# Optimization experiments

Hardware: AMD Instinct MI355X
Metric: run time of the kernel (lower is better)

## Reference

```python
import jax, jax.numpy as jnp
import numpy as np

BS, C, H, W = 4, 128, 64, 64  # input_dim=128
INNER = 64


def setup_inputs() -> dict:
    key = jax.random.key(0)
    ks = jax.random.split(key, 9)
    s_in = 1.0 / np.sqrt(C)
    s_inner = 1.0 / np.sqrt(INNER)
    return {
        "inpt": jax.random.normal(ks[0], (BS, C, H, W), dtype=jnp.float32),
        "Wq": jax.random.normal(ks[1], (INNER, C), dtype=jnp.float32) * s_in,
        "bq": jax.random.normal(ks[2], (INNER,), dtype=jnp.float32) * 0.01,
        "Wk": jax.random.normal(ks[3], (INNER, C), dtype=jnp.float32) * s_in,
        "bk": jax.random.normal(ks[4], (INNER,), dtype=jnp.float32) * 0.01,
        "Wv": jax.random.normal(ks[5], (INNER, C), dtype=jnp.float32) * s_in,
        "bv": jax.random.normal(ks[6], (INNER,), dtype=jnp.float32) * 0.01,
        "Wo": jax.random.normal(ks[7], (C, INNER), dtype=jnp.float32) * s_inner,
        "bo": jax.random.normal(ks[8], (C,), dtype=jnp.float32) * 0.01,
    }


def reference(inpt, Wq, bq, Wk, bk, Wv, bv, Wo, bo):
    bs, c, h, w = inpt.shape
    L = h * w
    # [bs, C, H, W] -> [bs, L, C] (tokens = spatial positions)
    x = inpt.reshape(bs, c, L).transpose(0, 2, 1)
    q = jnp.einsum('blc,dc->bld', x, Wq) + bq  # [bs, L, INNER]
    k = jnp.einsum('blc,dc->bld', x, Wk) + bk
    v = jnp.einsum('blc,dc->bld', x, Wv) + bv
    # torch code divides by np.round(sqrt(d), 2); for d=64 this is exactly 8.0
    scale = jnp.float32(np.round(np.sqrt(q.shape[-1]), 2))
    scores = jnp.einsum('bld,bmd->blm', q, k) / scale  # [bs, L, L] score matrix
    factors = jax.nn.softmax(scores, axis=-1)
    ctx = jnp.einsum('blm,bmd->bld', factors, v)  # [bs, L, INNER]
    out = jnp.einsum('bld,cd->blc', ctx, Wo) + bo  # [bs, L, C]
    out = out.transpose(0, 2, 1).reshape(bs, c, h, w)
    return inpt + out
```

## Files before the change

### kernel.cpp

```cpp
#include <hip/hip_runtime.h>
#include <hip/hip_bf16.h>

typedef __bf16 bf16x8 __attribute__((ext_vector_type(8)));
typedef __bf16 bf16x4 __attribute__((ext_vector_type(4)));
typedef short  s16x4  __attribute__((ext_vector_type(4)));
typedef float  f32x4  __attribute__((ext_vector_type(4)));

#define MFMA32(a, b, c) __builtin_amdgcn_mfma_f32_16x16x32_bf16((a), (b), (c), 0, 0, 0)
#define MFMA16K(a, b, c) __builtin_amdgcn_mfma_f32_16x16x16bf16_1k((a), (b), (c), 0, 0, 0)

#if __has_builtin(__builtin_amdgcn_exp2f)
#define EXP2F(x) __builtin_amdgcn_exp2f(x)
#else
#define EXP2F(x) __expf(0.6931471805599453f * (x))
#endif

#define GL16(G, L)                                                            \
    __builtin_amdgcn_global_load_lds(                                         \
        (const __attribute__((address_space(1))) void*)(G),                   \
        (__attribute__((address_space(3))) void*)(L), 16, 0, 0)

#define SPLIT 8
#define QSCALE 0.18033688011112042f
#define BBOUND 12.0f


__global__ __launch_bounds__(256) void wprep_kernel(
    const float* __restrict__ Wq, const float* __restrict__ Wk,
    const float* __restrict__ Wv, const float* __restrict__ Wo,
    __bf16* __restrict__ Wqkv_b, __bf16* __restrict__ Wo_b)
{
    const int idx = (blockIdx.x * 256 + threadIdx.x) * 4;
    const float* src;
    __bf16* dst;
    if (idx < 8192)       { src = Wq + idx;         dst = Wqkv_b + idx; }
    else if (idx < 16384) { src = Wk + idx - 8192;  dst = Wqkv_b + idx; }
    else if (idx < 24576) { src = Wv + idx - 16384; dst = Wqkv_b + idx; }
    else                  { src = Wo + idx - 24576; dst = Wo_b + idx - 24576; }
    float4 v = *(const float4*)src;
    bf16x4 o;
    o[0] = (__bf16)v.x; o[1] = (__bf16)v.y;
    o[2] = (__bf16)v.z; o[3] = (__bf16)v.w;
    *(bf16x4*)dst = o;
}

__global__ __launch_bounds__(256, 4) void qkv_kernel(
    const float* __restrict__ inpt,
    const float* __restrict__ bq, const float* __restrict__ bk,
    const float* __restrict__ bv,
    const __bf16* __restrict__ Wqkv_b,
    __bf16* __restrict__ Qws, __bf16* __restrict__ Kws, __bf16* __restrict__ VTws)
{
    __shared__ __align__(16) __bf16 xT[64 * 136];
    __shared__ __align__(16) __bf16 os[64 * 136];
    const int bid = blockIdx.x;
    const int b   = bid >> 6;
    const int l0  = (bid & 63) << 6;
    const int t   = threadIdx.x;

    {
        const int c = t >> 1, half = t & 1;
        const float* xin = inpt + ((size_t)(b * 128 + c)) * 4096 + l0 + half * 32;
        #pragma unroll
        for (int i = 0; i < 8; ++i) {
            float4 v = *(const float4*)(xin + i * 4);
            const int tok = half * 32 + i * 4;
            xT[(tok + 0) * 136 + c] = (__bf16)v.x;
            xT[(tok + 1) * 136 + c] = (__bf16)v.y;
            xT[(tok + 2) * 136 + c] = (__bf16)v.z;
            xT[(tok + 3) * 136 + c] = (__bf16)v.w;
        }
    }
    __syncthreads();

    const int w    = t >> 6;
    const int lane = t & 63;
    const int quad = lane >> 4;
    const int l15  = lane & 15;

    f32x4 acc[12];
    #pragma unroll
    for (int j = 0; j < 12; ++j)
        #pragma unroll
        for (int r = 0; r < 4; ++r) acc[j][r] = 0.f;

    #pragma unroll
    for (int ks = 0; ks < 4; ++ks) {
        bf16x8 af = *(const bf16x8*)&xT[(w * 16 + l15) * 136 + ks * 32 + quad * 8];
        #pragma unroll
        for (int j = 0; j < 12; ++j) {
            bf16x8 bf = *(const bf16x8*)(Wqkv_b + j * 2048 + l15 * 128
                                         + ks * 32 + quad * 8);
            acc[j] = MFMA32(af, bf, acc[j]);
        }
    }

    #pragma unroll
    for (int j = 0; j < 12; ++j) {
        const int msel = j >> 2;
        const int o0   = (j & 3) * 16;
        const float* bb = (msel == 0) ? bq : ((msel == 1) ? bk : bv);
        float bias = bb[o0 + l15];
        if (msel < 2) {
            const float scl = (msel == 0) ? QSCALE : 1.0f;
            const int oc = j * 16 + l15;
            #pragma unroll
            for (int r = 0; r < 4; ++r)
                os[(w * 16 + quad * 4 + r) * 136 + oc]
                    = (__bf16)((acc[j][r] + bias) * scl);
        } else {
            const int d  = o0 + l15;
            const int kt = bid & 63;
            bf16x4 v;
            #pragma unroll
            for (int r = 0; r < 4; ++r) v[r] = (__bf16)(acc[j][r] + bias);
            *(bf16x4*)(VTws + (size_t)b * 262144 + kt * 4096
                       + d * 64 + quad * 16 + w * 4) = v;
        }
    }
    __syncthreads();

    #pragma unroll
    for (int g = 0; g < 4; ++g) {
        const int cid = t + g * 256;
        const int tok = cid >> 4, c8 = cid & 15;
        bf16x8 v = *(const bf16x8*)&os[tok * 136 + c8 * 8];
        if (c8 < 8) {
            *(bf16x8*)(Qws + ((size_t)(b * 4096 + l0 + tok)) * 64 + c8 * 8) = v;
        } else {
            const int d8 = c8 - 8;
            __bf16* dst = Kws + (size_t)b * 262144
                + (bid & 63) * 4096
                + (tok >> 4) * 1024
                + (d8 >> 2) * 512
                + (d8 & 3) * 128
                + (tok & 15) * 8;
            *(bf16x8*)dst = v;
        }
    }
}

__global__ __launch_bounds__(256, 4) void attn_kernel(
    const __bf16* __restrict__ Qws, const __bf16* __restrict__ Kws,
    const __bf16* __restrict__ VTws,
    __bf16* __restrict__ Ops, float* __restrict__ Lws)
{
    __shared__ __align__(16) __bf16 sbuf[2][8192];

    const int bid0  = blockIdx.x;
    const int bid   = (bid0 & 7) * 128 + (bid0 >> 3);
    const int split = bid >> 7;
    const int qi    = bid & 127;
    const int b  = qi >> 5;
    const int l0 = (qi & 31) << 7;
    const int t    = threadIdx.x;
    const int w    = t >> 6;
    const int lane = t & 63;
    const int quad = lane >> 4;
    const int l15  = lane & 15;

    bf16x8 qf[2][2];
    #pragma unroll
    for (int qs = 0; qs < 2; ++qs) {
        const __bf16* qptr = Qws
            + ((size_t)(b * 4096 + l0 + w * 32 + qs * 16 + l15)) * 64 + quad * 8;
        qf[qs][0] = *(const bf16x8*)qptr;
        qf[qs][1] = *(const bf16x8*)(qptr + 32);
    }

    f32x4 cfr[2][4];
    #pragma unroll
    for (int qs = 0; qs < 2; ++qs)
        #pragma unroll
        for (int mt = 0; mt < 4; ++mt)
            #pragma unroll
            for (int r = 0; r < 4; ++r) cfr[qs][mt][r] = 0.f;
    float l_acc[2] = {0.f, 0.f};

    int voff[8];
    #pragma unroll
    for (int mt = 0; mt < 4; ++mt) {
        const int d = mt * 16 + l15;
        #pragma unroll
        for (int kc8 = 0; kc8 < 2; ++kc8)
            voff[kc8 * 4 + mt] = d * 64 + (((2 * quad + kc8) ^ (d & 7)) * 8);
    }

    const uint4* Vg = (const uint4*)(VTws + ((size_t)b << 18));
    const int rw = t >> 3, cw = (t & 7) ^ ((t >> 3) & 7);
    const uint4* vbase = Vg + rw * 8 + cw + split * 4096;
    const uint4* kbase = (const uint4*)(Kws + ((size_t)b << 18))
                       + t + split * 4096;

    union B4 { bf16x4 h; s16x4 s; };
    union V8 { bf16x8 v; s16x4 q[2]; };

    auto stage = [&](int kt, int slot) {
        __bf16* Kd = &sbuf[slot][0];
        __bf16* Vd = &sbuf[slot][4096];
        const uint4* kp = kbase + kt * 512;
        const uint4* vp = vbase + kt * 512;
        GL16(kp,       Kd +        w * 512);
        GL16(kp + 256, Kd + 2048 + w * 512);
        GL16(vp,       Vd +        w * 512);
        GL16(vp + 256, Vd + 2048 + w * 512);
    };

    auto tile_step = [&](int slot) {
        const __bf16* Kb = &sbuf[slot][0];
        const __bf16* Vb = &sbuf[slot][4096];
        B4 pk[2][4];
        #pragma unroll
        for (int nt = 0; nt < 4; ++nt) {
            bf16x8 k0 = *(const bf16x8*)(Kb + nt * 1024 +       lane * 8);
            bf16x8 k1 = *(const bf16x8*)(Kb + nt * 1024 + 512 + lane * 8);
            #pragma unroll
            for (int qs = 0; qs < 2; ++qs) {
                f32x4 a = {-BBOUND, -BBOUND, -BBOUND, -BBOUND};
                a = MFMA32(k0, qf[qs][0], a);
                a = MFMA32(k1, qf[qs][1], a);
                float p0 = EXP2F(a[0]), p1 = EXP2F(a[1]);
                float p2 = EXP2F(a[2]), p3 = EXP2F(a[3]);
                pk[qs][nt].h[0] = (__bf16)p0; pk[qs][nt].h[1] = (__bf16)p1;
                pk[qs][nt].h[2] = (__bf16)p2; pk[qs][nt].h[3] = (__bf16)p3;
                l_acc[qs] += (p0 + p1) + (p2 + p3);
            }
        }
        __builtin_amdgcn_s_setprio(1);
        #pragma unroll
        for (int kc8 = 0; kc8 < 2; ++kc8) {
            #pragma unroll
            for (int mt = 0; mt < 4; ++mt) {
                V8 vv;
                vv.v = *(const bf16x8*)&Vb[voff[kc8 * 4 + mt]];
                #pragma unroll
                for (int qs = 0; qs < 2; ++qs) {
                    cfr[qs][mt] = MFMA16K(vv.q[0], pk[qs][2 * kc8 + 0].s, cfr[qs][mt]);
                    cfr[qs][mt] = MFMA16K(vv.q[1], pk[qs][2 * kc8 + 1].s, cfr[qs][mt]);
                }
            }
        }
        __builtin_amdgcn_s_setprio(0);
    };

    stage(0, 0);
    for (int h = 0; h < 8; ++h) {
        asm volatile("s_waitcnt vmcnt(0)" ::: "memory");
        __builtin_amdgcn_s_barrier();
        asm volatile("" ::: "memory");
        if (h < 7) stage(h + 1, (h + 1) & 1);
        tile_step(h & 1);
    }

    __builtin_amdgcn_s_barrier();
    asm volatile("" ::: "memory");

    {
        __bf16* tb = (__bf16*)sbuf + w * 2176;
        #pragma unroll
        for (int qs = 0; qs < 2; ++qs)
            #pragma unroll
            for (int mt = 0; mt < 4; ++mt) {
                bf16x4 v;
                #pragma unroll
                for (int r = 0; r < 4; ++r) v[r] = (__bf16)cfr[qs][mt][r];
                *(bf16x4*)&tb[(qs * 16 + l15) * 68 + mt * 16 + quad * 4] = v;
            }
        const int rowbase = (split * 4 + b) * 4096 + l0 + w * 32;
        #pragma unroll
        for (int hh = 0; hh < 4; ++hh) {
            const int chunk = lane + hh * 64;
            const int tok = chunk >> 3, c8 = chunk & 7;
            bf16x8 v = *(const bf16x8*)&tb[tok * 68 + c8 * 8];
            *(bf16x8*)(Ops + (size_t)(rowbase + tok) * 64 + c8 * 8) = v;
        }
        #pragma unroll
        for (int qs = 0; qs < 2; ++qs) {
            float lr = l_acc[qs];
            lr += __shfl_xor(lr, 16);
            lr += __shfl_xor(lr, 32);
            if (quad == 0) Lws[rowbase + qs * 16 + l15] = lr;
        }
    }
}

__global__ __launch_bounds__(256, 4) void outproj_kernel(
    const float* __restrict__ inpt,
    const __bf16* __restrict__ Ops, const float* __restrict__ Lws,
    const __bf16* __restrict__ Wo_b, const float* __restrict__ bo,
    float* __restrict__ out)
{
    __shared__ __align__(16) __bf16 cx[64 * 72];
    const int bid = blockIdx.x;
    const int b   = bid >> 6;
    const int l0  = (bid & 63) << 6;
    const int t   = threadIdx.x;

    {
        const int token = t >> 2;
        const int rowb  = b * 4096 + l0 + token;
        float denom = 0.f;
        #pragma unroll
        for (int s = 0; s < SPLIT; ++s) denom += Lws[s * 16384 + rowb];
        const float inv = 1.f / denom;
        #pragma unroll
        for (int g = 0; g < 4; ++g) {
            const int d4 = (((t & 3) + g * 4)) << 2;
            float ax = 0.f, ay = 0.f, az = 0.f, aw = 0.f;
            #pragma unroll
            for (int s = 0; s < SPLIT; ++s) {
                const bf16x4 v = *(const bf16x4*)(Ops
                    + ((size_t)(s * 16384 + rowb)) * 64 + d4);
                ax += (float)v[0]; ay += (float)v[1];
                az += (float)v[2]; aw += (float)v[3];
            }
            bf16x4 pv;
            pv[0] = (__bf16)(ax * inv); pv[1] = (__bf16)(ay * inv);
            pv[2] = (__bf16)(az * inv); pv[3] = (__bf16)(aw * inv);
            *(bf16x4*)&cx[token * 72 + d4] = pv;
        }
    }
    __syncthreads();

    const int w    = t >> 6;
    const int lane = t & 63;
    const int quad = lane >> 4;
    const int l15  = lane & 15;

    f32x4 acc[2][4];
    #pragma unroll
    for (int mi = 0; mi < 2; ++mi)
        #pragma unroll
        for (int nt = 0; nt < 4; ++nt)
            #pragma unroll
            for (int r = 0; r < 4; ++r) acc[mi][nt][r] = 0.f;

    #pragma unroll
    for (int ks = 0; ks < 2; ++ks) {
        bf16x8 bfr[4];
        #pragma unroll
        for (int nt = 0; nt < 4; ++nt)
            bfr[nt] = *(const bf16x8*)&cx[(nt * 16 + l15) * 72 + ks * 32 + quad * 8];
        #pragma unroll
        for (int mi = 0; mi < 2; ++mi) {
            const int crow = (w * 2 + mi) * 16 + l15;
            bf16x8 af = *(const bf16x8*)(Wo_b + crow * 64 + ks * 32 + quad * 8);
            #pragma unroll
            for (int nt = 0; nt < 4; ++nt)
                acc[mi][nt] = MFMA32(af, bfr[nt], acc[mi][nt]);
        }
    }

    #pragma unroll
    for (int mi = 0; mi < 2; ++mi) {
        const int c0 = (w * 2 + mi) * 16 + quad * 4;
        #pragma unroll
        for (int nt = 0; nt < 4; ++nt) {
            #pragma unroll
            for (int r = 0; r < 4; ++r) {
                const int c = c0 + r;
                const size_t addr = ((size_t)(b * 128 + c)) * 4096
                                  + l0 + nt * 16 + l15;
                out[addr] = inpt[addr] + bo[c] + acc[mi][nt][r];
            }
        }
    }
}

extern "C" void kernel_launch(void* const* d_in, const int* in_sizes, int n_in,
                              void* d_out, int out_size, void* d_ws, size_t ws_size,
                              hipStream_t stream)
{
    const float* inpt = (const float*)d_in[0];
    const float* Wq   = (const float*)d_in[1];
    const float* bq   = (const float*)d_in[2];
    const float* Wk   = (const float*)d_in[3];
    const float* bk   = (const float*)d_in[4];
    const float* Wv   = (const float*)d_in[5];
    const float* bv   = (const float*)d_in[6];
    const float* Wo   = (const float*)d_in[7];
    const float* bo   = (const float*)d_in[8];
    float* out = (float*)d_out;

    char* ws = (char*)d_ws;
    const size_t MB = (size_t)1 << 20;
    __bf16* Qws    = (__bf16*)(ws + 0 * MB);
    __bf16* Kws    = (__bf16*)(ws + 2 * MB);
    __bf16* VTws   = (__bf16*)(ws + 4 * MB);
    __bf16* Ops    = (__bf16*)(ws + 6 * MB);
    float*  Lws    = (float*)(ws + 24 * MB);
    __bf16* Wqkv_b = (__bf16*)(ws + 25 * MB);
    __bf16* Wo_b   = (__bf16*)(ws + 25 * MB + (64 << 10));

    wprep_kernel<<<32, 256, 0, stream>>>(Wq, Wk, Wv, Wo, Wqkv_b, Wo_b);
    qkv_kernel<<<256, 256, 0, stream>>>(inpt, bq, bk, bv, Wqkv_b, Qws, Kws, VTws);
    attn_kernel<<<SPLIT * 128, 256, 0, stream>>>(Qws, Kws, VTws, Ops, Lws);
    outproj_kernel<<<256, 256, 0, stream>>>(inpt, Ops, Lws, Wo_b, bo, out);
}
```

Before: 118.7 us.

## Fold weight bf16 conversion into QKV and out-proj kernels, halve QKV tile

Removes the separate weight-prep kernel launch and converts fp32 weights to bf16 on the fly inside the QKV and output projection kernels. The QKV kernel now processes 32 tokens per block across 512 blocks, with the 4 waves split into 2 token halves × 2 output halves. This saves one launch and a global round trip but adds redundant fp32 weight loads and conversions in every block.

```diff
diff --git a/kernel.cpp b/kernel.cpp
--- a/kernel.cpp
+++ b/kernel.cpp
@@ -25,46 +25,28 @@
 #define BBOUND 12.0f
 
 
-__global__ __launch_bounds__(256) void wprep_kernel(
-    const float* __restrict__ Wq, const float* __restrict__ Wk,
-    const float* __restrict__ Wv, const float* __restrict__ Wo,
-    __bf16* __restrict__ Wqkv_b, __bf16* __restrict__ Wo_b)
-{
-    const int idx = (blockIdx.x * 256 + threadIdx.x) * 4;
-    const float* src;
-    __bf16* dst;
-    if (idx < 8192)       { src = Wq + idx;         dst = Wqkv_b + idx; }
-    else if (idx < 16384) { src = Wk + idx - 8192;  dst = Wqkv_b + idx; }
-    else if (idx < 24576) { src = Wv + idx - 16384; dst = Wqkv_b + idx; }
-    else                  { src = Wo + idx - 24576; dst = Wo_b + idx - 24576; }
-    float4 v = *(const float4*)src;
-    bf16x4 o;
-    o[0] = (__bf16)v.x; o[1] = (__bf16)v.y;
-    o[2] = (__bf16)v.z; o[3] = (__bf16)v.w;
-    *(bf16x4*)dst = o;
-}
-
 __global__ __launch_bounds__(256, 4) void qkv_kernel(
     const float* __restrict__ inpt,
-    const float* __restrict__ bq, const float* __restrict__ bk,
-    const float* __restrict__ bv,
-    const __bf16* __restrict__ Wqkv_b,
+    const float* __restrict__ Wq, const float* __restrict__ bq,
+    const float* __restrict__ Wk, const float* __restrict__ bk,
+    const float* __restrict__ Wv, const float* __restrict__ bv,
     __bf16* __restrict__ Qws, __bf16* __restrict__ Kws, __bf16* __restrict__ VTws)
 {
-    __shared__ __align__(16) __bf16 xT[64 * 136];
-    __shared__ __align__(16) __bf16 os[64 * 136];
-    const int bid = blockIdx.x;
-    const int b   = bid >> 6;
-    const int l0  = (bid & 63) << 6;
-    const int t   = threadIdx.x;
+    __shared__ __align__(16) __bf16 xT[32 * 136];
+    __shared__ __align__(16) __bf16 os[32 * 136];
+    const int bid  = blockIdx.x;
+    const int b    = bid >> 7;
+    const int tile = bid & 127;
+    const int l0   = tile << 5;
+    const int t    = threadIdx.x;
 
     {
         const int c = t >> 1, half = t & 1;
-        const float* xin = inpt + ((size_t)(b * 128 + c)) * 4096 + l0 + half * 32;
-        #pragma unroll
-        for (int i = 0; i < 8; ++i) {
+        const float* xin = inpt + ((size_t)(b * 128 + c)) * 4096 + l0 + half * 16;
+        #pragma unroll
+        for (int i = 0; i < 4; ++i) {
             float4 v = *(const float4*)(xin + i * 4);
-            const int tok = half * 32 + i * 4;
+            const int tok = half * 16 + i * 4;
             xT[(tok + 0) * 136 + c] = (__bf16)v.x;
             xT[(tok + 1) * 136 + c] = (__bf16)v.y;
             xT[(tok + 2) * 136 + c] = (__bf16)v.z;
@@ -77,26 +59,39 @@
     const int lane = t & 63;
     const int quad = lane >> 4;
     const int l15  = lane & 15;
-
-    f32x4 acc[12];
-    #pragma unroll
-    for (int j = 0; j < 12; ++j)
-        #pragma unroll
-        for (int r = 0; r < 4; ++r) acc[j][r] = 0.f;
+    const int tw   = w & 1;
+    const int jh   = w >> 1;
+
+    f32x4 acc[6];
+    #pragma unroll
+    for (int jj = 0; jj < 6; ++jj)
+        #pragma unroll
+        for (int r = 0; r < 4; ++r) acc[jj][r] = 0.f;
 
     #pragma unroll
     for (int ks = 0; ks < 4; ++ks) {
-        bf16x8 af = *(const bf16x8*)&xT[(w * 16 + l15) * 136 + ks * 32 + quad * 8];
-        #pragma unroll
-        for (int j = 0; j < 12; ++j) {
-            bf16x8 bf = *(const bf16x8*)(Wqkv_b + j * 2048 + l15 * 128
-                                         + ks * 32 + quad * 8);
-            acc[j] = MFMA32(af, bf, acc[j]);
-        }
-    }
-
-    #pragma unroll
-    for (int j = 0; j < 12; ++j) {
+        bf16x8 af = *(const bf16x8*)&xT[(tw * 16 + l15) * 136 + ks * 32 + quad * 8];
+        #pragma unroll
+        for (int jj = 0; jj < 6; ++jj) {
+            const int j    = jh * 6 + jj;
+            const int msel = j >> 2;
+            const float* W = (msel == 0) ? Wq : ((msel == 1) ? Wk : Wv);
+            const float* Wp = W + ((j & 3) * 16 + l15) * 128 + ks * 32 + quad * 8;
+            float4 wa = *(const float4*)Wp;
+            float4 wb = *(const float4*)(Wp + 4);
+            bf16x8 bf;
+            bf[0] = (__bf16)wa.x; bf[1] = (__bf16)wa.y;
+            bf[2] = (__bf16)wa.z; bf[3] = (__bf16)wa.w;
+            bf[4] = (__bf16)wb.x; bf[5] = (__bf16)wb.y;
+            bf[6] = (__bf16)wb.z; bf[7] = (__bf16)wb.w;
+            acc[jj] = MFMA32(af, bf, acc[jj]);
+        }
+    }
+
+    const int T16 = tile * 2 + tw;
+    #pragma unroll
+    for (int jj = 0; jj < 6; ++jj) {
+        const int j    = jh * 6 + jj;
         const int msel = j >> 2;
         const int o0   = (j & 3) * 16;
         const float* bb = (msel == 0) ? bq : ((msel == 1) ? bk : bv);
@@ -106,32 +101,34 @@
             const int oc = j * 16 + l15;
             #pragma unroll
             for (int r = 0; r < 4; ++r)
-                os[(w * 16 + quad * 4 + r) * 136 + oc]
-                    = (__bf16)((acc[j][r] + bias) * scl);
+                os[(tw * 16 + quad * 4 + r) * 136 + oc]
+                    = (__bf16)((acc[jj][r] + bias) * scl);
         } else {
             const int d  = o0 + l15;
-            const int kt = bid & 63;
+            const int kt = T16 >> 2;
+            const int kc = T16 & 3;
             bf16x4 v;
             #pragma unroll
-            for (int r = 0; r < 4; ++r) v[r] = (__bf16)(acc[j][r] + bias);
+            for (int r = 0; r < 4; ++r) v[r] = (__bf16)(acc[jj][r] + bias);
             *(bf16x4*)(VTws + (size_t)b * 262144 + kt * 4096
-                       + d * 64 + quad * 16 + w * 4) = v;
+                       + d * 64 + quad * 16 + kc * 4) = v;
         }
     }
     __syncthreads();
 
     #pragma unroll
-    for (int g = 0; g < 4; ++g) {
+    for (int g = 0; g < 2; ++g) {
         const int cid = t + g * 256;
         const int tok = cid >> 4, c8 = cid & 15;
         bf16x8 v = *(const bf16x8*)&os[tok * 136 + c8 * 8];
         if (c8 < 8) {
             *(bf16x8*)(Qws + ((size_t)(b * 4096 + l0 + tok)) * 64 + c8 * 8) = v;
         } else {
-            const int d8 = c8 - 8;
+            const int d8   = c8 - 8;
+            const int KT16 = tile * 2 + (tok >> 4);
             __bf16* dst = Kws + (size_t)b * 262144
-                + (bid & 63) * 4096
-                + (tok >> 4) * 1024
+                + (KT16 >> 2) * 4096
+                + (KT16 & 3) * 1024
                 + (d8 >> 2) * 512
                 + (d8 & 3) * 128
                 + (tok & 15) * 8;
@@ -287,7 +284,7 @@
 __global__ __launch_bounds__(256, 4) void outproj_kernel(
     const float* __restrict__ inpt,
     const __bf16* __restrict__ Ops, const float* __restrict__ Lws,
-    const __bf16* __restrict__ Wo_b, const float* __restrict__ bo,
+    const float* __restrict__ Wo, const float* __restrict__ bo,
     float* __restrict__ out)
 {
     __shared__ __align__(16) __bf16 cx[64 * 72];
@@ -344,7 +341,14 @@
         #pragma unroll
         for (int mi = 0; mi < 2; ++mi) {
             const int crow = (w * 2 + mi) * 16 + l15;
-            bf16x8 af = *(const bf16x8*)(Wo_b + crow * 64 + ks * 32 + quad * 8);
+            const float* Wp = Wo + crow * 64 + ks * 32 + quad * 8;
+            float4 wa = *(const float4*)Wp;
+            float4 wb = *(const float4*)(Wp + 4);
+            bf16x8 af;
+            af[0] = (__bf16)wa.x; af[1] = (__bf16)wa.y;
+            af[2] = (__bf16)wa.z; af[3] = (__bf16)wa.w;
+            af[4] = (__bf16)wb.x; af[5] = (__bf16)wb.y;
+            af[6] = (__bf16)wb.z; af[7] = (__bf16)wb.w;
             #pragma unroll
             for (int nt = 0; nt < 4; ++nt)
                 acc[mi][nt] = MFMA32(af, bfr[nt], acc[mi][nt]);
@@ -389,11 +393,9 @@
     __bf16* VTws   = (__bf16*)(ws + 4 * MB);
     __bf16* Ops    = (__bf16*)(ws + 6 * MB);
     float*  Lws    = (float*)(ws + 24 * MB);
-    __bf16* Wqkv_b = (__bf16*)(ws + 25 * MB);
-    __bf16* Wo_b   = (__bf16*)(ws + 25 * MB + (64 << 10));
-
-    wprep_kernel<<<32, 256, 0, stream>>>(Wq, Wk, Wv, Wo, Wqkv_b, Wo_b);
-    qkv_kernel<<<256, 256, 0, stream>>>(inpt, bq, bk, bv, Wqkv_b, Qws, Kws, VTws);
+
+    qkv_kernel<<<512, 256, 0, stream>>>(inpt, Wq, bq, Wk, bk, Wv, bv,
+                                        Qws, Kws, VTws);
     attn_kernel<<<SPLIT * 128, 256, 0, stream>>>(Qws, Kws, VTws, Ops, Lws);
-    outproj_kernel<<<256, 256, 0, stream>>>(inpt, Ops, Lws, Wo_b, bo, out);
+    outproj_kernel<<<256, 256, 0, stream>>>(inpt, Ops, Lws, Wo, bo, out);
 }
```

Result: slower. 123.2 us (+3.8%).
